# Kernel tuning notes

Hardware: AMD Instinct MI355X
Metric: run time of the kernel (lower is better)

Reference implementation:

```python
import jax, jax.numpy as jnp
import numpy as np
from jax import lax

DIM = 192
HEADS = 4
HIDDEN = int(DIM * 2.66)  # 510


def _conv1x1(x, w, b):
    # x: [B,C,H,W], w: [O,C], b: [O]
    return jnp.einsum('bchw,oc->bohw', x, w) + b[None, :, None, None]


def _dwconv3x3(x, w, b):
    # x: [B,C,H,W], w: [C,1,3,3], b: [C]
    c = x.shape[1]
    y = lax.conv_general_dilated(x, w, window_strides=(1, 1), padding='SAME',
                                 feature_group_count=c,
                                 dimension_numbers=('NCHW', 'OIHW', 'NCHW'))
    return y + b[None, :, None, None]


def _layernorm_c(x, w, b):
    # LayerNorm over channel dim (torch LayerNorm(dim) applied to b,(hw),c)
    mu = jnp.mean(x, axis=1, keepdims=True)
    var = jnp.mean((x - mu) ** 2, axis=1, keepdims=True)
    xn = (x - mu) / jnp.sqrt(var + 1e-5)
    return xn * w[None, :, None, None] + b[None, :, None, None]


def _l2norm(x):
    # F.normalize(dim=-1), eps=1e-12
    n = jnp.sqrt(jnp.sum(x * x, axis=-1, keepdims=True))
    return x / jnp.maximum(n, 1e-12)


def setup_inputs() -> dict:
    key = jax.random.key(0)
    ks = jax.random.split(key, 16)
    s = 0.02
    d, h2 = DIM, HIDDEN * 2
    return {
        'x': jax.random.normal(ks[0], (4, DIM, 128, 128), jnp.float32),
        'ln1_w': jnp.ones((d,), jnp.float32),
        'ln1_b': jnp.zeros((d,), jnp.float32),
        'qkv_w': jax.random.normal(ks[1], (3 * d, d), jnp.float32) * s,
        'qkv_b': jnp.zeros((3 * d,), jnp.float32),
        'qkv_dw_w': jax.random.normal(ks[2], (3 * d, 1, 3, 3), jnp.float32) * s,
        'qkv_dw_b': jnp.zeros((3 * d,), jnp.float32),
        'temperature': jnp.ones((HEADS, 1, 1), jnp.float32),
        'proj_w': jax.random.normal(ks[3], (d, d), jnp.float32) * s,
        'proj_b': jnp.zeros((d,), jnp.float32),
        'ln2_w': jnp.ones((d,), jnp.float32),
        'ln2_b': jnp.zeros((d,), jnp.float32),
        'pin_w': jax.random.normal(ks[4], (h2, d), jnp.float32) * s,
        'pin_b': jnp.zeros((h2,), jnp.float32),
        'dw_w': jax.random.normal(ks[5], (h2, 1, 3, 3), jnp.float32) * s,
        'dw_b': jnp.zeros((h2,), jnp.float32),
        'pout_w': jax.random.normal(ks[6], (d, HIDDEN), jnp.float32) * s,
        'pout_b': jnp.zeros((d,), jnp.float32),
    }


def _attention(x, qkv_w, qkv_b, qkv_dw_w, qkv_dw_b, temperature, proj_w, proj_b):
    b, c, h, w = x.shape
    qkv = _dwconv3x3(_conv1x1(x, qkv_w, qkv_b), qkv_dw_w, qkv_dw_b)
    q, k, v = jnp.split(qkv, 3, axis=1)
    ch = c // HEADS

    def heads(t):  # b (head c) h w -> b head c (h w)
        return t.reshape(b, HEADS, ch, h * w)

    q, k, v = heads(q), heads(k), heads(v)
    q = _l2norm(q)
    k = _l2norm(k)
    attn = jnp.einsum('bhcn,bhdn->bhcd', q, k) * temperature[None]  # [b,H,ch,ch]
    attn = jax.nn.softmax(attn, axis=-1)
    out = jnp.einsum('bhcd,bhdn->bhcn', attn, v)
    out = out.reshape(b, c, h, w)
    return _conv1x1(out, proj_w, proj_b)


def _ffn(x, pin_w, pin_b, dw_w, dw_b, pout_w, pout_b):
    y = _conv1x1(x, pin_w, pin_b)
    y = _dwconv3x3(y, dw_w, dw_b)
    x1, x2 = jnp.split(y, 2, axis=1)
    y = jax.nn.gelu(x1, approximate=False) * x2
    return _conv1x1(y, pout_w, pout_b)


def reference(x, ln1_w, ln1_b, qkv_w, qkv_b, qkv_dw_w, qkv_dw_b, temperature,
              proj_w, proj_b, ln2_w, ln2_b, pin_w, pin_b, dw_w, dw_b,
              pout_w, pout_b):
    x = x + _attention(_layernorm_c(x, ln1_w, ln1_b), qkv_w, qkv_b,
                       qkv_dw_w, qkv_dw_b, temperature, proj_w, proj_b)
    x = x + _ffn(_layernorm_c(x, ln2_w, ln2_b), pin_w, pin_b, dw_w, dw_b,
                 pout_w, pout_b)
    return x
```

## Files before the change

kernel.cpp:

```cpp
#include <hip/hip_runtime.h>
#include <math.h>

typedef long long i64;
typedef unsigned short u16;
typedef unsigned int u32;

#define HW 16384
#define DIM 192
#define NHEADS 4
#define CH 48
#define OQKV 576
#define HID 510
#define H2 1020
#define NB 4
#define NSPLIT 64
#define QKSTR 264

typedef __attribute__((ext_vector_type(8))) short short8v;
typedef __attribute__((ext_vector_type(4))) float float4v;

__device__ __forceinline__ u32 pk(float a, float b) {
  u32 r;
  asm("v_cvt_pk_bf16_f32 %0, %1, %2" : "=v"(r) : "v"(a), "v"(b));
  return r;
}
__device__ __forceinline__ u16 f2bf(float f) {
  union { float f; u32 u; } v; v.f = f;
  u32 r = v.u + 0x7FFF + ((v.u >> 16) & 1);
  return (u16)(r >> 16);
}
__device__ __forceinline__ float bflo(u32 w) {
  union { u32 u; float f; } v; v.u = w << 16; return v.f;
}
__device__ __forceinline__ float bfhi(u32 w) {
  union { u32 u; float f; } v; v.u = w & 0xFFFF0000u; return v.f;
}
__device__ __forceinline__ float bf1(u16 h) {
  union { u32 u; float f; } v; v.u = ((u32)h) << 16; return v.f;
}
__device__ __forceinline__ float gelu_s(float x) {
  return x / (1.f + __expf(-1.702f * x));
}

#define GLL16(gp, lp) __builtin_amdgcn_global_load_lds( \
    (const __attribute__((address_space(1))) u32*)(gp), \
    (__attribute__((address_space(3))) u32*)(lp), 16, 0, 0)

__global__ __launch_bounds__(256) void ln_kernel(const float* __restrict__ x,
    const float* __restrict__ w, const float* __restrict__ b, u16* __restrict__ yT) {
  __shared__ float st[32][193];
  __shared__ float red[2][8][32];
  __shared__ float murs[2][32];
  const float* xb = x + (i64)blockIdx.y * DIM * HW;
  u16* yb = yT + (i64)blockIdx.y * (i64)HW * DIM;
  int tid = threadIdx.x;
  int g = tid >> 5, p = tid & 31;
  int pix0 = blockIdx.x * 32;
  float s = 0.f, ss = 0.f;
  #pragma unroll
  for (int i = 0; i < 24; ++i) {
    float t = xb[(i64)(g * 24 + i) * HW + pix0 + p];
    st[p][g * 24 + i] = t; s += t; ss += t * t;
  }
  red[0][g][p] = s; red[1][g][p] = ss;
  __syncthreads();
  if (tid < 32) {
    float S = 0.f, SS = 0.f;
    #pragma unroll
    for (int gg = 0; gg < 8; ++gg) { S += red[0][gg][tid]; SS += red[1][gg][tid]; }
    float mu = S * (1.f / DIM);
    float var = SS * (1.f / DIM) - mu * mu;
    murs[0][tid] = mu;
    murs[1][tid] = rsqrtf(var + 1e-5f);
  }
  __syncthreads();
  int px = tid >> 3, c0 = (tid & 7) * 24;
  float mu = murs[0][px], rs = murs[1][px];
  u32 ob[12];
  #pragma unroll
  for (int i = 0; i < 24; i += 2) {
    float va = (st[px][c0 + i + 0] - mu) * rs * w[c0 + i + 0] + b[c0 + i + 0];
    float vb = (st[px][c0 + i + 1] - mu) * rs * w[c0 + i + 1] + b[c0 + i + 1];
    ob[i >> 1] = pk(va, vb);
  }
  u16* yp = yb + (i64)(pix0 + px) * DIM + c0;
  #pragma unroll
  for (int j = 0; j < 3; ++j) *(uint4*)(yp + j * 8) = *(const uint4*)&ob[j * 4];
}

__global__ __launch_bounds__(256) void wconv_all(const float* __restrict__ qkv_w,
    const float* __restrict__ proj_w, const float* __restrict__ pin_w,
    const float* __restrict__ pout_w, u16* __restrict__ Wq, u16* __restrict__ Wpj,
    u16* __restrict__ Wpi, u16* __restrict__ Wpo) {
  int idx = blockIdx.x * 256 + threadIdx.x;
  const float* src; u16* dst; int O, C, Kpad;
  if (idx < 122880)      { src = qkv_w;  dst = Wq;  O = OQKV; C = 192; Kpad = 192; }
  else if (idx < 172032) { idx -= 122880; src = proj_w; dst = Wpj; O = 192;  C = 192; Kpad = 192; }
  else if (idx < 368640) { idx -= 172032; src = pin_w;  dst = Wpi; O = H2;   C = 192; Kpad = 192; }
  else if (idx < 499712) { idx -= 368640; src = pout_w; dst = Wpo; O = 192;  C = HID; Kpad = 512; }
  else return;
  int r = idx / Kpad, c = idx - r * Kpad;
  dst[idx] = f2bf((r < O && c < C) ? src[(i64)r * C + c] : 0.f);
}

__global__ __launch_bounds__(256) void gemm_bf16(const u16* __restrict__ A,
    const float* __restrict__ bias, const u16* __restrict__ B,
    const float* __restrict__ Res, float* __restrict__ Out,
    u16* __restrict__ OutB, int O, int K, i64 sB, i64 sOut, i64 sRes) {
  __shared__ __align__(16) u16 lds[2 * 128 * 64];
  int zb = blockIdx.z;
  B += (i64)zb * sB;
  if (Res) Res += (i64)zb * sRes;
  if (OutB) OutB += (i64)zb * sOut; else Out += (i64)zb * sOut;
  int tid = threadIdx.x;
  int lane = tid & 63, wave = tid >> 6;
  int wm = (wave >> 1) * 64, wn = (wave & 1) * 64;
  int obase = blockIdx.y * 128, nbase = blockIdx.x * 128;
  float4v acc[4][4];
  #pragma unroll
  for (int m = 0; m < 4; ++m)
    #pragma unroll
    for (int n = 0; n < 4; ++n) acc[m][n] = (float4v){0.f, 0.f, 0.f, 0.f};

  const u16* Abase = A + (i64)obase * K;
  const u16* Bbase = B + (i64)nbase * K;
  char* ldsA = (char*)&lds[0];
  char* ldsB = (char*)&lds[8192];
  int srow = wave * 8 + (lane >> 3);
  int sj = lane & 7;

  for (int k0 = 0; k0 < K; k0 += 64) {
    #pragma unroll
    for (int iss = 0; iss < 4; ++iss) {
      int r = iss * 32 + srow;
      int kb = sj ^ (r & 7);
      GLL16(Abase + (i64)r * K + k0 + kb * 8, ldsA + iss * 4096 + wave * 1024);
      GLL16(Bbase + (i64)r * K + k0 + kb * 8, ldsB + iss * 4096 + wave * 1024);
    }
    __syncthreads();
    #pragma unroll
    for (int kk = 0; kk < 2; ++kk) {
      short8v af[4], bfr[4];
      #pragma unroll
      for (int m = 0; m < 4; ++m) {
        int r = wm + m * 16 + (lane & 15);
        int kb = kk * 4 + (lane >> 4);
        af[m] = *(const short8v*)(ldsA + r * 128 + ((kb ^ (r & 7)) << 4));
      }
      #pragma unroll
      for (int n = 0; n < 4; ++n) {
        int r = wn + n * 16 + (lane & 15);
        int kb = kk * 4 + (lane >> 4);
        bfr[n] = *(const short8v*)(ldsB + r * 128 + ((kb ^ (r & 7)) << 4));
      }
      #pragma unroll
      for (int m = 0; m < 4; ++m)
        #pragma unroll
        for (int n = 0; n < 4; ++n)
          acc[m][n] = __builtin_amdgcn_mfma_f32_16x16x32_bf16(af[m], bfr[n], acc[m][n], 0, 0, 0);
    }
    __syncthreads();
  }

  int rowq = lane >> 4, coln = lane & 15;
  if (OutB) {
    #pragma unroll
    for (int m = 0; m < 4; ++m) {
      #pragma unroll
      for (int reg = 0; reg < 4; ++reg) {
        int o = wm + m * 16 + rowq * 4 + reg;
        int oo = obase + o;
        float bv = (oo < O) ? bias[oo] : 0.f;
        #pragma unroll
        for (int n = 0; n < 4; n += 2) {
          u32 w2 = pk(acc[m][n][reg] + bv, acc[m][n + 1][reg] + bv);
          lds[o * 128 + wn + n * 16 + coln] = (u16)w2;
          lds[o * 128 + wn + (n + 1) * 16 + coln] = (u16)(w2 >> 16);
        }
      }
    }
    __syncthreads();
    const u32* st32 = (const u32*)lds;
    #pragma unroll
    for (int k = 0; k < 32; ++k) {
      int idx = k * 256 + tid;
      int o = idx >> 6, cd = idx & 63;
      if (obase + o < O)
        ((u32*)(OutB + (i64)(obase + o) * HW + nbase))[cd] = st32[o * 64 + cd];
    }
  } else {
    #pragma unroll
    for (int m = 0; m < 4; ++m) {
      #pragma unroll
      for (int reg = 0; reg < 4; ++reg) {
        int o = obase + wm + m * 16 + rowq * 4 + reg;
        if (o >= O) continue;
        float bv = bias[o];
        #pragma unroll
        for (int n = 0; n < 4; ++n) {
          int nn = nbase + wn + n * 16 + coln;
          float v = acc[m][n][reg] + bv;
          if (Res) v += Res[(i64)o * HW + nn];
          Out[(i64)o * HW + nn] = v;
        }
      }
    }
  }
}

__global__ __launch_bounds__(256) void dwconv_bf16(const u16* __restrict__ in,
    const float* __restrict__ w9, const float* __restrict__ bs,
    u16* __restrict__ out) {
  in  += (i64)blockIdx.z * OQKV * HW;
  out += (i64)blockIdx.z * OQKV * HW;
  int q = threadIdx.x & 31;
  int grp = threadIdx.x >> 5;
  int y0 = blockIdx.y * 2;
  int c0 = blockIdx.x * 64 + grp * 8;
  int xb = q * 4;
  #pragma unroll
  for (int i = 0; i < 8; ++i) {
    int c = c0 + i;
    const float* wp = w9 + c * 9;
    float bv = bs[c];
    const u16* chan = in + (i64)c * HW;
    float f[4][6];
    #pragma unroll
    for (int r4 = 0; r4 < 4; ++r4) {
      int yy = y0 - 1 + r4;
      if (yy < 0 || yy >= 128) {
        #pragma unroll
        for (int e = 0; e < 6; ++e) f[r4][e] = 0.f;
      } else {
        uint4 raw = *(const uint4*)(chan + yy * 128 + xb - 2);
        f[r4][0] = (q == 0) ? 0.f : bfhi(raw.x);
        f[r4][1] = bflo(raw.y); f[r4][2] = bfhi(raw.y);
        f[r4][3] = bflo(raw.z); f[r4][4] = bfhi(raw.z);
        f[r4][5] = (q == 31) ? 0.f : bflo(raw.w);
      }
    }
    #pragma unroll
    for (int rr = 0; rr < 2; ++rr) {
      float a0 = bv, a1 = bv, a2 = bv, a3 = bv;
      #pragma unroll
      for (int dy = 0; dy < 3; ++dy) {
        float wa = wp[dy * 3 + 0], wb = wp[dy * 3 + 1], wc = wp[dy * 3 + 2];
        const float* fr = f[rr + dy];
        a0 += wa * fr[0] + wb * fr[1] + wc * fr[2];
        a1 += wa * fr[1] + wb * fr[2] + wc * fr[3];
        a2 += wa * fr[2] + wb * fr[3] + wc * fr[4];
        a3 += wa * fr[3] + wb * fr[4] + wc * fr[5];
      }
      uint2 o2;
      o2.x = pk(a0, a1);
      o2.y = pk(a2, a3);
      *(uint2*)(out + (i64)c * HW + (y0 + rr) * 128 + xb) = o2;
    }
  }
}

__global__ __launch_bounds__(256) void l2inv_bf16(const u16* __restrict__ qkv,
    float* __restrict__ inv) {
  int ch = blockIdx.x;
  const u16* p = qkv + (i64)blockIdx.y * OQKV * HW + (i64)ch * HW;
  float s = 0.f;
  for (int i = threadIdx.x * 8; i < HW; i += 256 * 8) {
    uint4 raw = *(const uint4*)(p + i);
    float v0 = bflo(raw.x), v1 = bfhi(raw.x);
    float v2 = bflo(raw.y), v3 = bfhi(raw.y);
    float v4 = bflo(raw.z), v5 = bfhi(raw.z);
    float v6 = bflo(raw.w), v7 = bfhi(raw.w);
    s += v0 * v0 + v1 * v1 + v2 * v2 + v3 * v3 + v4 * v4 + v5 * v5 + v6 * v6 + v7 * v7;
  }
  #pragma unroll
  for (int m = 32; m; m >>= 1) s += __shfl_xor(s, m);
  __shared__ float wsum[4];
  int lane = threadIdx.x & 63, wid = threadIdx.x >> 6;
  if (lane == 0) wsum[wid] = s;
  __syncthreads();
  if (threadIdx.x == 0) {
    float t = wsum[0] + wsum[1] + wsum[2] + wsum[3];
    inv[(i64)blockIdx.y * 384 + ch] = 1.f / fmaxf(sqrtf(t), 1e-12f);
  }
}

__global__ __launch_bounds__(256) void attn_qk_mfma(const u16* __restrict__ qkv,
    float* __restrict__ part) {
  qkv  += (i64)blockIdx.z * OQKV * HW;
  part += (i64)blockIdx.z * 589824;
  __shared__ __align__(16) u16 qs[48][QKSTR];
  __shared__ __align__(16) u16 ks[48][QKSTR];
  int h = blockIdx.x, spb = blockIdx.y;
  int n0 = spb * 1024;
  const u16* qb = qkv + (i64)(h * CH) * HW;
  const u16* kb = qkv + (i64)(DIM + h * CH) * HW;
  int tid = threadIdx.x;
  int lane = tid & 63, wave = tid >> 6;
  float4v acc[3][3];
  #pragma unroll
  for (int i = 0; i < 3; ++i)
    #pragma unroll
    for (int j = 0; j < 3; ++j) acc[i][j] = (float4v){0.f, 0.f, 0.f, 0.f};

  for (int it = 0; it < 4; ++it) {
    int base = n0 + it * 256;
    for (int l = tid; l < 1536; l += 256) {
      int r = l >> 5, j = (l & 31) * 8;
      *(uint4*)&qs[r][j] = *(const uint4*)(qb + (i64)r * HW + base + j);
      *(uint4*)&ks[r][j] = *(const uint4*)(kb + (i64)r * HW + base + j);
    }
    __syncthreads();
    int kbase = wave * 64;
    #pragma unroll
    for (int ksi = 0; ksi < 2; ++ksi) {
      int kofs = kbase + ksi * 32 + (lane >> 4) * 8;
      short8v aq[3], bk[3];
      #pragma unroll
      for (int t = 0; t < 3; ++t) {
        aq[t] = *(const short8v*)&qs[t * 16 + (lane & 15)][kofs];
        bk[t] = *(const short8v*)&ks[t * 16 + (lane & 15)][kofs];
      }
      #pragma unroll
      for (int ci = 0; ci < 3; ++ci)
        #pragma unroll
        for (int di = 0; di < 3; ++di)
          acc[ci][di] = __builtin_amdgcn_mfma_f32_16x16x32_bf16(aq[ci], bk[di], acc[ci][di], 0, 0, 0);
    }
    __syncthreads();
  }
  int rowq = lane >> 4, coln = lane & 15;
  float* pp = part + ((i64)(h * NSPLIT) + spb * 4 + wave) * 2304;
  #pragma unroll
  for (int ci = 0; ci < 3; ++ci)
    #pragma unroll
    for (int reg = 0; reg < 4; ++reg) {
      int c = ci * 16 + rowq * 4 + reg;
      #pragma unroll
      for (int di = 0; di < 3; ++di)
        pp[c * 48 + di * 16 + coln] = acc[ci][di][reg];
    }
}

__global__ __launch_bounds__(64) void attn_sm3(const float* __restrict__ part,
    const float* __restrict__ inv, const float* __restrict__ temp,
    float* __restrict__ attn) {
  part += (i64)blockIdx.z * 589824;
  attn += (i64)blockIdx.z * 9216;
  const float* invb = inv + (i64)blockIdx.z * 384;
  int h = blockIdx.x, c = blockIdx.y;
  int d = threadIdx.x;
  float logit = -1e30f;
  if (d < CH) {
    float s = 0.f;
    for (int sp = 0; sp < NSPLIT; ++sp)
      s += part[((i64)(h * NSPLIT) + sp) * 2304 + c * 48 + d];
    logit = s * invb[h * CH + c] * invb[192 + h * CH + d] * temp[h];
  }
  float m = logit;
  #pragma unroll
  for (int mask = 32; mask; mask >>= 1) m = fmaxf(m, __shfl_xor(m, mask));
  float e = (d < CH) ? expf(logit - m) : 0.f;
  float ssum = e;
  #pragma unroll
  for (int mask = 32; mask; mask >>= 1) ssum += __shfl_xor(ssum, mask);
  if (d < CH) attn[(i64)h * 2304 + c * 48 + d] = e / ssum;
}

__global__ __launch_bounds__(256) void attn_v_kernel(const u16* __restrict__ qkv,
    const float* __restrict__ attnm, u16* __restrict__ outT) {
  qkv   += (i64)blockIdx.z * OQKV * HW;
  attnm += (i64)blockIdx.z * 9216;
  outT  += (i64)blockIdx.z * (i64)HW * DIM;
  __shared__ float as[CH * CH];
  __shared__ u16 st[256 * 52];
  int h = blockIdx.x, tile = blockIdx.y;
  int tid = threadIdx.x;
  for (int l = tid; l < CH * CH; l += 256) as[l] = attnm[(i64)h * 2304 + l];
  __syncthreads();
  int n = tile * 256 + tid;
  const u16* vb = qkv + (i64)(2 * DIM + h * CH) * HW + n;
  float vreg[CH];
  #pragma unroll
  for (int d = 0; d < CH; ++d) vreg[d] = bf1(vb[(i64)d * HW]);
  u32* strow = (u32*)st + tid * 26;
  #pragma unroll 2
  for (int c = 0; c < CH; c += 4) {
    float a0 = 0.f, a1 = 0.f, a2 = 0.f, a3 = 0.f;
    const float* r0 = &as[(c + 0) * CH];
    const float* r1 = &as[(c + 1) * CH];
    const float* r2 = &as[(c + 2) * CH];
    const float* r3 = &as[(c + 3) * CH];
    #pragma unroll
    for (int d = 0; d < CH; ++d) {
      float vv = vreg[d];
      a0 += r0[d] * vv; a1 += r1[d] * vv; a2 += r2[d] * vv; a3 += r3[d] * vv;
    }
    strow[(c >> 1) + 0] = pk(a0, a1);
    strow[(c >> 1) + 1] = pk(a2, a3);
  }
  __syncthreads();
  const uint2* sv = (const uint2*)st;
  u16* ob = outT + (i64)(tile * 256) * DIM + h * CH;
  #pragma unroll
  for (int k = 0; k < 12; ++k) {
    int idx = k * 256 + tid;
    int px = idx / 12, pc = idx - px * 12;
    *(uint2*)(ob + (i64)px * DIM + pc * 4) = sv[px * 13 + pc];
  }
}

__global__ __launch_bounds__(256) void dwgate_bf16(const u16* __restrict__ h1,
    const float* __restrict__ w9, const float* __restrict__ bs,
    u16* __restrict__ og) {
  h1 += (i64)blockIdx.z * H2 * HW;
  og += (i64)blockIdx.z * (i64)HW * 512;
  __shared__ u32 st[128 * 17];
  int q = threadIdx.x & 31;
  int grp = threadIdx.x >> 5;
  int y = blockIdx.y;
  int c0 = blockIdx.x * 32 + grp * 4;
  int xb = q * 4;
  float prev[4];
  #pragma unroll
  for (int i = 0; i < 4; ++i) {
    int c = c0 + i;
    bool valid = (c < HID);
    float b1 = valid ? bs[c] : 0.f;
    float b2 = valid ? bs[c + HID] : 0.f;
    float a0 = b1, a1 = b1, a2 = b1, a3 = b1;
    float g0 = b2, g1 = b2, g2 = b2, g3 = b2;
    if (valid) {
      const float* wp1 = w9 + c * 9;
      const float* wp2 = w9 + (i64)(c + HID) * 9;
      const u16* ch1 = h1 + (i64)c * HW;
      const u16* ch2 = h1 + (i64)(c + HID) * HW;
      #pragma unroll
      for (int dy = -1; dy <= 1; ++dy) {
        int yy = y + dy;
        if (yy < 0 || yy >= 128) continue;
        {
          uint4 raw = *(const uint4*)(ch1 + yy * 128 + xb - 2);
          float f1 = bfhi(raw.x);
          float f2 = bflo(raw.y), f3 = bfhi(raw.y);
          float f4 = bflo(raw.z), f5 = bfhi(raw.z);
          float f6 = bflo(raw.w);
          if (q == 0) f1 = 0.f;
          if (q == 31) f6 = 0.f;
          float wa = wp1[(dy + 1) * 3 + 0], wb = wp1[(dy + 1) * 3 + 1], wc = wp1[(dy + 1) * 3 + 2];
          a0 += wa * f1 + wb * f2 + wc * f3;
          a1 += wa * f2 + wb * f3 + wc * f4;
          a2 += wa * f3 + wb * f4 + wc * f5;
          a3 += wa * f4 + wb * f5 + wc * f6;
        }
        {
          uint4 raw = *(const uint4*)(ch2 + yy * 128 + xb - 2);
          float f1 = bfhi(raw.x);
          float f2 = bflo(raw.y), f3 = bfhi(raw.y);
          float f4 = bflo(raw.z), f5 = bfhi(raw.z);
          float f6 = bflo(raw.w);
          if (q == 0) f1 = 0.f;
          if (q == 31) f6 = 0.f;
          float wa = wp2[(dy + 1) * 3 + 0], wb = wp2[(dy + 1) * 3 + 1], wc = wp2[(dy + 1) * 3 + 2];
          g0 += wa * f1 + wb * f2 + wc * f3;
          g1 += wa * f2 + wb * f3 + wc * f4;
          g2 += wa * f3 + wb * f4 + wc * f5;
          g3 += wa * f4 + wb * f5 + wc * f6;
        }
      }
    }
    float r0 = valid ? gelu_s(a0) * g0 : 0.f;
    float r1 = valid ? gelu_s(a1) * g1 : 0.f;
    float r2 = valid ? gelu_s(a2) * g2 : 0.f;
    float r3 = valid ? gelu_s(a3) * g3 : 0.f;
    if (i & 1) {
      int dwi = grp * 2 + (i >> 1);
      st[(xb + 0) * 17 + dwi] = pk(prev[0], r0);
      st[(xb + 1) * 17 + dwi] = pk(prev[1], r1);
      st[(xb + 2) * 17 + dwi] = pk(prev[2], r2);
      st[(xb + 3) * 17 + dwi] = pk(prev[3], r3);
    } else {
      prev[0] = r0; prev[1] = r1; prev[2] = r2; prev[3] = r3;
    }
  }
  __syncthreads();
  u32* og32 = (u32*)og;
  int tid = threadIdx.x;
  #pragma unroll
  for (int k = 0; k < 8; ++k) {
    int idx = k * 256 + tid;
    int px = idx >> 4, dwi = idx & 15;
    og32[(i64)(y * 128 + px) * 256 + blockIdx.x * 16 + dwi] = st[px * 17 + dwi];
  }
}

extern "C" void kernel_launch(void* const* d_in, const int* in_sizes, int n_in,
                              void* d_out, int out_size, void* d_ws, size_t ws_size,
                              hipStream_t stream) {
  const float* x        = (const float*)d_in[0];
  const float* ln1_w    = (const float*)d_in[1];
  const float* ln1_b    = (const float*)d_in[2];
  const float* qkv_w    = (const float*)d_in[3];
  const float* qkv_b    = (const float*)d_in[4];
  const float* qkv_dw_w = (const float*)d_in[5];
  const float* qkv_dw_b = (const float*)d_in[6];
  const float* temp     = (const float*)d_in[7];
  const float* proj_w   = (const float*)d_in[8];
  const float* proj_b   = (const float*)d_in[9];
  const float* ln2_w    = (const float*)d_in[10];
  const float* ln2_b    = (const float*)d_in[11];
  const float* pin_w    = (const float*)d_in[12];
  const float* pin_b    = (const float*)d_in[13];
  const float* dw_w     = (const float*)d_in[14];
  const float* dw_b     = (const float*)d_in[15];
  const float* pout_w   = (const float*)d_in[16];
  const float* pout_b   = (const float*)d_in[17];
  float* out = (float*)d_out;
  char* ws = (char*)d_ws;

  u16* Wq   = (u16*)ws;
  u16* Wpj  = Wq + 640 * 192;
  u16* Wpi  = Wpj + 256 * 192;
  u16* Wpo  = Wpi + 1024 * 192;
  u16* yT   = Wpo + 256 * 512;
  char* dyn = (char*)(yT + (i64)NB * HW * DIM);

  auto layout = [&](int nb, float*& attnm, float*& part, float*& invv,
                    u16*& bufA, u16*& bufQ) -> size_t {
    char* p = dyn;
    attnm = (float*)p; p += (i64)nb * 9216 * 4;
    part  = (float*)p; p += (i64)nb * 589824 * 4;
    invv  = (float*)p; p += (i64)nb * 384 * 4;
    bufA  = (u16*)p;   p += (i64)nb * H2 * HW * 2;
    bufQ  = (u16*)p;   p += (i64)nb * OQKV * HW * 2;
    return (size_t)(p - ws);
  };

  float *attnm, *part, *invv; u16 *bufA, *bufQ;
  int nbat = 4;
  if (layout(4, attnm, part, invv, bufA, bufQ) > ws_size) {
    nbat = 1;
    if (layout(1, attnm, part, invv, bufA, bufQ) > ws_size) return;
  }

  wconv_all<<<(499712 + 255) / 256, 256, 0, stream>>>(qkv_w, proj_w, pin_w, pout_w,
                                                      Wq, Wpj, Wpi, Wpo);
  ln_kernel<<<dim3(HW / 32, NB), 256, 0, stream>>>(x, ln1_w, ln1_b, yT);

  for (int b0 = 0; b0 < NB; b0 += nbat) {
    const float* xb = x + (i64)b0 * DIM * HW;
    float* outb = out + (i64)b0 * DIM * HW;
    u16* yTb = yT + (i64)b0 * HW * DIM;
    u16* attnoutT = bufA;
    u16* gatedT = bufQ;

    gemm_bf16<<<dim3(HW / 128, 5, nbat), 256, 0, stream>>>(
        Wq, qkv_b, yTb, nullptr, nullptr, bufA, OQKV, DIM,
        (i64)HW * DIM, (i64)OQKV * HW, 0);
    dwconv_bf16<<<dim3(OQKV / 64, 64, nbat), 256, 0, stream>>>(bufA, qkv_dw_w, qkv_dw_b, bufQ);
    l2inv_bf16<<<dim3(384, nbat), 256, 0, stream>>>(bufQ, invv);
    attn_qk_mfma<<<dim3(NHEADS, 16, nbat), 256, 0, stream>>>(bufQ, part);
    attn_sm3<<<dim3(NHEADS, CH, nbat), 64, 0, stream>>>(part, invv, temp, attnm);
    attn_v_kernel<<<dim3(NHEADS, HW / 256, nbat), 256, 0, stream>>>(bufQ, attnm, attnoutT);
    gemm_bf16<<<dim3(HW / 128, 2, nbat), 256, 0, stream>>>(
        Wpj, proj_b, attnoutT, xb, outb, nullptr, DIM, DIM,
        (i64)HW * DIM, (i64)DIM * HW, (i64)DIM * HW);

    ln_kernel<<<dim3(HW / 32, nbat), 256, 0, stream>>>(outb, ln2_w, ln2_b, yTb);
    gemm_bf16<<<dim3(HW / 128, 8, nbat), 256, 0, stream>>>(
        Wpi, pin_b, yTb, nullptr, nullptr, bufA, H2, DIM,
        (i64)HW * DIM, (i64)H2 * HW, 0);
    dwgate_bf16<<<dim3(16, 128, nbat), 256, 0, stream>>>(bufA, dw_w, dw_b, gatedT);
    gemm_bf16<<<dim3(HW / 128, 2, nbat), 256, 0, stream>>>(
        Wpo, pout_b, gatedT, outb, outb, nullptr, DIM, 512,
        (i64)HW * 512, (i64)DIM * HW, (i64)DIM * HW);
  }
}
```

Before: 474.8 us.

## Add skinny single-wave MFMA GEMM for 192-output projection layers

Adds a 64-thread kernel in which each wave computes all 192 output channels for 32 pixels. A and B fragments are read directly from global memory with no LDS staging, and the kernel uses it for the attention projection and FFN output GEMMs in place of the tiled gemm_bf16 with two output blocks. The goal is to avoid splitting the 192 outputs across blocks, which re-reads the activation matrix, and to drop LDS and sync overhead. In exchange it holds 24 accumulators per lane, giving high register pressure, uses uncoalesced strided global loads, and has small 64-thread blocks.

```diff
diff --git a/kernel.cpp b/kernel.cpp
--- a/kernel.cpp
+++ b/kernel.cpp
@@ -203,6 +203,51 @@
           if (Res) v += Res[(i64)o * HW + nn];
           Out[(i64)o * HW + nn] = v;
         }
+      }
+    }
+  }
+}
+
+__global__ __launch_bounds__(64) void gemm_skinny(const u16* __restrict__ A,
+    const float* __restrict__ bias, const u16* __restrict__ B,
+    const float* __restrict__ Res, float* __restrict__ Out,
+    int K, i64 sB, i64 sOut, i64 sRes) {
+  int zb = blockIdx.y;
+  B   += (i64)zb * sB;
+  Res += (i64)zb * sRes;
+  Out += (i64)zb * sOut;
+  int lane = threadIdx.x;
+  int r = lane & 15, kq = lane >> 4;
+  int nbase = blockIdx.x * 32;
+  float4v acc[12][2];
+  #pragma unroll
+  for (int mi = 0; mi < 12; ++mi) {
+    acc[mi][0] = (float4v){0.f, 0.f, 0.f, 0.f};
+    acc[mi][1] = (float4v){0.f, 0.f, 0.f, 0.f};
+  }
+  const u16* Ap = A + (i64)r * K + kq * 8;
+  const u16* Bp0 = B + (i64)(nbase + r) * K + kq * 8;
+  const u16* Bp1 = Bp0 + (i64)16 * K;
+  for (int ks = 0; ks < K; ks += 32) {
+    short8v b0 = *(const short8v*)(Bp0 + ks);
+    short8v b1 = *(const short8v*)(Bp1 + ks);
+    #pragma unroll
+    for (int mi = 0; mi < 12; ++mi) {
+      short8v a = *(const short8v*)(Ap + (i64)mi * 16 * K + ks);
+      acc[mi][0] = __builtin_amdgcn_mfma_f32_16x16x32_bf16(a, b0, acc[mi][0], 0, 0, 0);
+      acc[mi][1] = __builtin_amdgcn_mfma_f32_16x16x32_bf16(a, b1, acc[mi][1], 0, 0, 0);
+    }
+  }
+  #pragma unroll
+  for (int mi = 0; mi < 12; ++mi) {
+    #pragma unroll
+    for (int reg = 0; reg < 4; ++reg) {
+      int o = mi * 16 + kq * 4 + reg;
+      float bv = bias[o];
+      #pragma unroll
+      for (int ni = 0; ni < 2; ++ni) {
+        int n = nbase + ni * 16 + r;
+        Out[(i64)o * HW + n] = acc[mi][ni][reg] + bv + Res[(i64)o * HW + n];
       }
     }
   }
@@ -561,8 +606,8 @@
     attn_qk_mfma<<<dim3(NHEADS, 16, nbat), 256, 0, stream>>>(bufQ, part);
     attn_sm3<<<dim3(NHEADS, CH, nbat), 64, 0, stream>>>(part, invv, temp, attnm);
     attn_v_kernel<<<dim3(NHEADS, HW / 256, nbat), 256, 0, stream>>>(bufQ, attnm, attnoutT);
-    gemm_bf16<<<dim3(HW / 128, 2, nbat), 256, 0, stream>>>(
-        Wpj, proj_b, attnoutT, xb, outb, nullptr, DIM, DIM,
+    gemm_skinny<<<dim3(HW / 32, nbat), 64, 0, stream>>>(
+        Wpj, proj_b, attnoutT, xb, outb, DIM,
         (i64)HW * DIM, (i64)DIM * HW, (i64)DIM * HW);
 
     ln_kernel<<<dim3(HW / 32, nbat), 256, 0, stream>>>(outb, ln2_w, ln2_b, yTb);
@@ -570,8 +615,8 @@
         Wpi, pin_b, yTb, nullptr, nullptr, bufA, H2, DIM,
         (i64)HW * DIM, (i64)H2 * HW, 0);
     dwgate_bf16<<<dim3(16, 128, nbat), 256, 0, stream>>>(bufA, dw_w, dw_b, gatedT);
-    gemm_bf16<<<dim3(HW / 128, 2, nbat), 256, 0, stream>>>(
-        Wpo, pout_b, gatedT, outb, outb, nullptr, DIM, 512,
+    gemm_skinny<<<dim3(HW / 32, nbat), 64, 0, stream>>>(
+        Wpo, pout_b, gatedT, outb, outb, 512,
         (i64)HW * 512, (i64)DIM * HW, (i64)DIM * HW);
   }
 }
```

Result: faster. 436.1 us (-8.2%).
